# Kernel tuning notes

Hardware: AMD Instinct MI355X
Metric: run time of the kernel (lower is better)

## Reference

```python
import jax, jax.numpy as jnp
import numpy as np

TARGET_SIZE = 1024
SOURCE_SIZE = 1024


def setup_inputs() -> dict:
    key = jax.random.key(0)
    k1, k2, k3, k4 = jax.random.split(key, 4)
    B, T, S = 16, 1024, 1024
    sentence_state = jax.random.normal(k1, (B, T, TARGET_SIZE), dtype=jnp.float32)
    graph_state = jax.random.normal(k2, (B, S, SOURCE_SIZE), dtype=jnp.float32)
    mask = jax.random.bernoulli(k3, 0.5, (B, T, S))  # bool
    # nn.Linear(target_size+source_size, 1, bias=False).weight flattened
    w = jax.random.normal(k4, (TARGET_SIZE + SOURCE_SIZE,), dtype=jnp.float32) * (
        1.0 / np.sqrt(TARGET_SIZE + SOURCE_SIZE)
    )
    return {"sentence_state": sentence_state, "graph_state": graph_state, "mask": mask, "w": w}


def reference(sentence_state, graph_state, mask, w):
    # Linear on concat([tgt, src]) with out_features=1 decomposes into two dot products:
    # score[b,t,s] = sentence[b,t,:] @ w_t + graph[b,s,:] @ w_s
    w_t = w[:TARGET_SIZE]
    w_s = w[TARGET_SIZE:]
    st = jnp.einsum("btd,d->bt", sentence_state, w_t)  # (B, T)
    gs = jnp.einsum("bsd,d->bs", graph_state, w_s)  # (B, S)
    scores = st[:, :, None] + gs[:, None, :]  # (B, T, S)
    attn = jax.nn.softmax(scores, axis=-1)
    attn = attn * (~mask).astype(attn.dtype)
    norm = jnp.sum(attn, axis=-1, keepdims=True) + 1e-12
    return attn / norm
```

## Files before the change

### kernel.cpp

```cpp
#include <hip/hip_runtime.h>


constexpr int Bb = 16;
constexpr int Tt = 1024;
constexpr int Ss = 1024;
constexpr int Dd = 1024;

__global__ __launch_bounds__(256) void gs_exp_probe_kernel(
    const float* __restrict__ graph, const float* __restrict__ w_full,
    const unsigned char* __restrict__ mask, int* __restrict__ ws_flag,
    float* __restrict__ e_out) {
  if (blockIdx.x == 0) {
    __shared__ int nz[4];
    const int tid = threadIdx.x;
    if (tid < 4) nz[tid] = 0;
    __syncthreads();
    uchar4 v = reinterpret_cast<const uchar4*>(mask)[tid];
    if (v.x) atomicOr(&nz[0], 1);
    if (v.y) atomicOr(&nz[1], 1);
    if (v.z) atomicOr(&nz[2], 1);
    if (v.w) atomicOr(&nz[3], 1);
    __syncthreads();
    if (tid == 0) {
      int spread = (nz[0] != 0) + (nz[1] != 0) + (nz[2] != 0) + (nz[3] != 0);
      ws_flag[0] = (spread >= 3) ? 0 : 1;
    }
  }

  const int lane = threadIdx.x & 63;
  const int wv   = threadIdx.x >> 6;
  const long row = (long)blockIdx.x * 4 + wv;
  const float4* r  = reinterpret_cast<const float4*>(graph) + row * (Dd / 4);
  const float4* ws = reinterpret_cast<const float4*>(w_full + 1024);
  float acc = 0.f;
#pragma unroll
  for (int k = 0; k < 4; ++k) {
    float4 a = r[lane + 64 * k];
    float4 b = ws[lane + 64 * k];
    acc = fmaf(a.x, b.x, acc);
    acc = fmaf(a.y, b.y, acc);
    acc = fmaf(a.z, b.z, acc);
    acc = fmaf(a.w, b.w, acc);
  }
#pragma unroll
  for (int off = 32; off; off >>= 1) acc += __shfl_xor(acc, off, 64);
  if (lane == 0) e_out[row] = __expf(acc);
}

__global__ __launch_bounds__(256) void PointerGenerator_9259949490200_kernel(
    const float* __restrict__ e, const unsigned char* __restrict__ mask,
    const int* __restrict__ ws_flag, float* __restrict__ out) {
  constexpr int ROWS = 2;
  const int lane = threadIdx.x & 63;
  const int wv   = threadIdx.x >> 6;
  const int b    = blockIdx.y;

  const float4* e4 = reinterpret_cast<const float4*>(e + (long)b * Ss);
  float4 pr[4];
#pragma unroll
  for (int k = 0; k < 4; ++k) pr[k] = e4[lane + 64 * k];

  const int  mode = ws_flag[0];
  const long t0   = (long)blockIdx.x * (4 * ROWS) + (long)wv * ROWS;
  const long row0 = (long)b * Tt + t0;

  unsigned int mw[ROWS][4];
  if (mode == 0) {
    const unsigned int* m4 =
        reinterpret_cast<const unsigned int*>(mask + row0 * Ss);
#pragma unroll
    for (int r = 0; r < ROWS; ++r)
#pragma unroll
      for (int k = 0; k < 4; ++k) mw[r][k] = m4[r * 256 + lane + 64 * k];
  } else {
    const int4* m4 = reinterpret_cast<const int4*>(
        reinterpret_cast<const int*>(mask) + row0 * Ss);
#pragma unroll
    for (int r = 0; r < ROWS; ++r)
#pragma unroll
      for (int k = 0; k < 4; ++k) {
        int4 w = m4[r * 256 + lane + 64 * k];
        mw[r][k] = (unsigned)(w.x != 0) | ((unsigned)(w.y != 0) << 8) |
                   ((unsigned)(w.z != 0) << 16) | ((unsigned)(w.w != 0) << 24);
      }
  }

  float sum[ROWS];
#pragma unroll
  for (int r = 0; r < ROWS; ++r) {
    float s = 0.f;
#pragma unroll
    for (int k = 0; k < 4; ++k) {
      const unsigned int m = mw[r][k];
      s += (m & 0x000000FFu) ? 0.f : pr[k].x;
      s += (m & 0x0000FF00u) ? 0.f : pr[k].y;
      s += (m & 0x00FF0000u) ? 0.f : pr[k].z;
      s += (m & 0xFF000000u) ? 0.f : pr[k].w;
    }
    sum[r] = s;
  }
#pragma unroll
  for (int off = 32; off; off >>= 1)
#pragma unroll
    for (int r = 0; r < ROWS; ++r) sum[r] += __shfl_xor(sum[r], off, 64);

#pragma unroll
  for (int r = 0; r < ROWS; ++r) {
    const float invD = 1.0f / (sum[r] + 1e-12f);
    float4* orow = reinterpret_cast<float4*>(out + (row0 + r) * Ss);
#pragma unroll
    for (int k = 0; k < 4; ++k) {
      const unsigned int m = mw[r][k];
      float4 v;
      v.x = (m & 0x000000FFu) ? 0.f : pr[k].x * invD;
      v.y = (m & 0x0000FF00u) ? 0.f : pr[k].y * invD;
      v.z = (m & 0x00FF0000u) ? 0.f : pr[k].z * invD;
      v.w = (m & 0xFF000000u) ? 0.f : pr[k].w * invD;
      orow[lane + 64 * k] = v;
    }
  }
}

extern "C" void kernel_launch(void* const* d_in, const int* in_sizes, int n_in,
                              void* d_out, int out_size, void* d_ws, size_t ws_size,
                              hipStream_t stream) {
  const float* graph        = (const float*)d_in[1];
  const unsigned char* mask = (const unsigned char*)d_in[2];
  const float* w            = (const float*)d_in[3];
  float* out = (float*)d_out;

  int*   ws_flag = (int*)d_ws;
  float* e       = (float*)((char*)d_ws + 256);

  gs_exp_probe_kernel<<<(Bb * Ss) / 4, 256, 0, stream>>>(graph, w, mask,
                                                         ws_flag, e);
  PointerGenerator_9259949490200_kernel<<<dim3(Tt / (4 * 2), Bb), 256, 0, stream>>>(
      e, mask, ws_flag, out);
}
```

Baseline: 35.85 us.

## Fuse graph-score and normalize kernels with producer/consumer waves and spin-wait flags

Result: slower. 54.25 us (+51.3%).

```diff
diff --git a/kernel.cpp b/kernel.cpp
--- a/kernel.cpp
+++ b/kernel.cpp
@@ -6,117 +6,125 @@
 constexpr int Ss = 1024;
 constexpr int Dd = 1024;
 
-__global__ __launch_bounds__(256) void gs_exp_probe_kernel(
+__global__ __launch_bounds__(256) void zero_e_kernel(float* __restrict__ e) {
+  reinterpret_cast<float4*>(e)[blockIdx.x * 256 + threadIdx.x] =
+      make_float4(0.f, 0.f, 0.f, 0.f);
+}
+
+__global__ __launch_bounds__(256, 2) void PointerGenerator_9259949490200_kernel(
     const float* __restrict__ graph, const float* __restrict__ w_full,
-    const unsigned char* __restrict__ mask, int* __restrict__ ws_flag,
-    float* __restrict__ e_out) {
-  if (blockIdx.x == 0) {
-    __shared__ int nz[4];
-    const int tid = threadIdx.x;
-    if (tid < 4) nz[tid] = 0;
-    __syncthreads();
-    uchar4 v = reinterpret_cast<const uchar4*>(mask)[tid];
-    if (v.x) atomicOr(&nz[0], 1);
-    if (v.y) atomicOr(&nz[1], 1);
-    if (v.z) atomicOr(&nz[2], 1);
-    if (v.w) atomicOr(&nz[3], 1);
-    __syncthreads();
-    if (tid == 0) {
-      int spread = (nz[0] != 0) + (nz[1] != 0) + (nz[2] != 0) + (nz[3] != 0);
-      ws_flag[0] = (spread >= 3) ? 0 : 1;
-    }
-  }
-
+    const unsigned char* __restrict__ mask, float* e, float* __restrict__ out) {
   const int lane = threadIdx.x & 63;
   const int wv   = threadIdx.x >> 6;
-  const long row = (long)blockIdx.x * 4 + wv;
-  const float4* r  = reinterpret_cast<const float4*>(graph) + row * (Dd / 4);
-  const float4* ws = reinterpret_cast<const float4*>(w_full + 1024);
-  float acc = 0.f;
+  const int blk  = blockIdx.x;
+
+  if (wv < 2) {
+    const float4* wsv = reinterpret_cast<const float4*>(w_full + Ss);
+    float4 wr[4];
 #pragma unroll
-  for (int k = 0; k < 4; ++k) {
-    float4 a = r[lane + 64 * k];
-    float4 b = ws[lane + 64 * k];
-    acc = fmaf(a.x, b.x, acc);
-    acc = fmaf(a.y, b.y, acc);
-    acc = fmaf(a.z, b.z, acc);
-    acc = fmaf(a.w, b.w, acc);
-  }
-#pragma unroll
-  for (int off = 32; off; off >>= 1) acc += __shfl_xor(acc, off, 64);
-  if (lane == 0) e_out[row] = __expf(acc);
-}
-
-__global__ __launch_bounds__(256) void PointerGenerator_9259949490200_kernel(
-    const float* __restrict__ e, const unsigned char* __restrict__ mask,
-    const int* __restrict__ ws_flag, float* __restrict__ out) {
-  constexpr int ROWS = 2;
-  const int lane = threadIdx.x & 63;
-  const int wv   = threadIdx.x >> 6;
-  const int b    = blockIdx.y;
-
-  const float4* e4 = reinterpret_cast<const float4*>(e + (long)b * Ss);
-  float4 pr[4];
-#pragma unroll
-  for (int k = 0; k < 4; ++k) pr[k] = e4[lane + 64 * k];
-
-  const int  mode = ws_flag[0];
-  const long t0   = (long)blockIdx.x * (4 * ROWS) + (long)wv * ROWS;
-  const long row0 = (long)b * Tt + t0;
-
-  unsigned int mw[ROWS][4];
-  if (mode == 0) {
-    const unsigned int* m4 =
-        reinterpret_cast<const unsigned int*>(mask + row0 * Ss);
-#pragma unroll
-    for (int r = 0; r < ROWS; ++r)
-#pragma unroll
-      for (int k = 0; k < 4; ++k) mw[r][k] = m4[r * 256 + lane + 64 * k];
-  } else {
-    const int4* m4 = reinterpret_cast<const int4*>(
-        reinterpret_cast<const int*>(mask) + row0 * Ss);
-#pragma unroll
-    for (int r = 0; r < ROWS; ++r)
+    for (int k = 0; k < 4; ++k) wr[k] = wsv[lane + 64 * k];
+    const int rbase = blk * 2 + wv;
+#pragma unroll 1
+    for (int b = 0; b < Bb; ++b) {
+      const long row = (long)b * Ss + rbase;
+      const float4* r = reinterpret_cast<const float4*>(graph) + row * (Dd / 4);
+      float acc = 0.f;
 #pragma unroll
       for (int k = 0; k < 4; ++k) {
-        int4 w = m4[r * 256 + lane + 64 * k];
-        mw[r][k] = (unsigned)(w.x != 0) | ((unsigned)(w.y != 0) << 8) |
-                   ((unsigned)(w.z != 0) << 16) | ((unsigned)(w.w != 0) << 24);
+        float4 a = r[lane + 64 * k];
+        acc = fmaf(a.x, wr[k].x, acc);
+        acc = fmaf(a.y, wr[k].y, acc);
+        acc = fmaf(a.z, wr[k].z, acc);
+        acc = fmaf(a.w, wr[k].w, acc);
       }
-  }
+#pragma unroll
+      for (int off = 32; off; off >>= 1) acc += __shfl_xor(acc, off, 64);
+      if (lane == 0)
+        __hip_atomic_store(&e[row], __expf(acc), __ATOMIC_RELAXED,
+                           __HIP_MEMORY_SCOPE_AGENT);
+    }
+  } else {
+    uint4 pv = reinterpret_cast<const uint4*>(mask)[lane];
+    int bits = 0;
+    {
+      unsigned dw[4] = {pv.x, pv.y, pv.z, pv.w};
+#pragma unroll
+      for (int j = 0; j < 4; ++j) {
+        unsigned d = dw[j];
+        bits |= ((d & 0x000000FFu) ? 1 : 0) | ((d & 0x0000FF00u) ? 2 : 0) |
+                ((d & 0x00FF0000u) ? 4 : 0) | ((d & 0xFF000000u) ? 8 : 0);
+      }
+    }
+    const int spread = ((__ballot(bits & 1) != 0ull) ? 1 : 0) +
+                       ((__ballot(bits & 2) != 0ull) ? 1 : 0) +
+                       ((__ballot(bits & 4) != 0ull) ? 1 : 0) +
+                       ((__ballot(bits & 8) != 0ull) ? 1 : 0);
+    const int mode = (spread >= 3) ? 0 : 1;
+    const int trow = blk * 2 + (wv - 2);
 
-  float sum[ROWS];
+#pragma unroll 1
+    for (int b = 0; b < Bb; ++b) {
+      const float* eb = e + (long)b * Ss;
+      float ev[16];
+      int tries = 0;
+      while (true) {
+        bool ok = true;
 #pragma unroll
-  for (int r = 0; r < ROWS; ++r) {
-    float s = 0.f;
+        for (int k = 0; k < 4; ++k)
 #pragma unroll
-    for (int k = 0; k < 4; ++k) {
-      const unsigned int m = mw[r][k];
-      s += (m & 0x000000FFu) ? 0.f : pr[k].x;
-      s += (m & 0x0000FF00u) ? 0.f : pr[k].y;
-      s += (m & 0x00FF0000u) ? 0.f : pr[k].z;
-      s += (m & 0xFF000000u) ? 0.f : pr[k].w;
-    }
-    sum[r] = s;
-  }
+          for (int c = 0; c < 4; ++c) {
+            float v = __hip_atomic_load(&eb[4 * lane + 256 * k + c],
+                                        __ATOMIC_RELAXED,
+                                        __HIP_MEMORY_SCOPE_AGENT);
+            ev[4 * k + c] = v;
+            ok = ok && (v > 0.f);
+          }
+        if (__all(ok) || ++tries > 200000) break;
+        __builtin_amdgcn_s_sleep(8);
+      }
+
+      const long orow = (long)b * Tt + trow;
+      unsigned mw[4];
+      if (mode == 0) {
+        const unsigned* mr =
+            reinterpret_cast<const unsigned*>(mask + orow * Ss);
 #pragma unroll
-  for (int off = 32; off; off >>= 1)
+        for (int k = 0; k < 4; ++k) mw[k] = mr[lane + 64 * k];
+      } else {
+        const int4* mr = reinterpret_cast<const int4*>(
+            reinterpret_cast<const int*>(mask) + orow * Ss);
 #pragma unroll
-    for (int r = 0; r < ROWS; ++r) sum[r] += __shfl_xor(sum[r], off, 64);
+        for (int k = 0; k < 4; ++k) {
+          int4 w = mr[lane + 64 * k];
+          mw[k] = (unsigned)(w.x != 0) | ((unsigned)(w.y != 0) << 8) |
+                  ((unsigned)(w.z != 0) << 16) | ((unsigned)(w.w != 0) << 24);
+        }
+      }
 
+      float s = 0.f;
 #pragma unroll
-  for (int r = 0; r < ROWS; ++r) {
-    const float invD = 1.0f / (sum[r] + 1e-12f);
-    float4* orow = reinterpret_cast<float4*>(out + (row0 + r) * Ss);
+      for (int k = 0; k < 4; ++k) {
+        const unsigned m = mw[k];
+        s += (m & 0x000000FFu) ? 0.f : ev[4 * k + 0];
+        s += (m & 0x0000FF00u) ? 0.f : ev[4 * k + 1];
+        s += (m & 0x00FF0000u) ? 0.f : ev[4 * k + 2];
+        s += (m & 0xFF000000u) ? 0.f : ev[4 * k + 3];
+      }
 #pragma unroll
-    for (int k = 0; k < 4; ++k) {
-      const unsigned int m = mw[r][k];
-      float4 v;
-      v.x = (m & 0x000000FFu) ? 0.f : pr[k].x * invD;
-      v.y = (m & 0x0000FF00u) ? 0.f : pr[k].y * invD;
-      v.z = (m & 0x00FF0000u) ? 0.f : pr[k].z * invD;
-      v.w = (m & 0xFF000000u) ? 0.f : pr[k].w * invD;
-      orow[lane + 64 * k] = v;
+      for (int off = 32; off; off >>= 1) s += __shfl_xor(s, off, 64);
+      const float invD = 1.0f / (s + 1e-12f);
+
+      float4* o = reinterpret_cast<float4*>(out + orow * Ss);
+#pragma unroll
+      for (int k = 0; k < 4; ++k) {
+        const unsigned m = mw[k];
+        float4 v;
+        v.x = (m & 0x000000FFu) ? 0.f : ev[4 * k + 0] * invD;
+        v.y = (m & 0x0000FF00u) ? 0.f : ev[4 * k + 1] * invD;
+        v.z = (m & 0x00FF0000u) ? 0.f : ev[4 * k + 2] * invD;
+        v.w = (m & 0xFF000000u) ? 0.f : ev[4 * k + 3] * invD;
+        o[lane + 64 * k] = v;
+      }
     }
   }
 }
@@ -128,12 +136,9 @@
   const unsigned char* mask = (const unsigned char*)d_in[2];
   const float* w            = (const float*)d_in[3];
   float* out = (float*)d_out;
+  float* e   = (float*)d_ws;
 
-  int*   ws_flag = (int*)d_ws;
-  float* e       = (float*)((char*)d_ws + 256);
-
-  gs_exp_probe_kernel<<<(Bb * Ss) / 4, 256, 0, stream>>>(graph, w, mask,
-                                                         ws_flag, e);
-  PointerGenerator_9259949490200_kernel<<<dim3(Tt / (4 * 2), Bb), 256, 0, stream>>>(
-      e, mask, ws_flag, out);
+  zero_e_kernel<<<16, 256, 0, stream>>>(e);
+  PointerGenerator_9259949490200_kernel<<<512, 256, 0, stream>>>(
+      graph, w, mask, e, out);
 }
```

## Split row-sum normalization into a separate kernel before output write

Applied to the files above, without the earlier changes.

Result: slower. 47.53 us (+32.6%).

```diff
diff --git a/kernel.cpp b/kernel.cpp
--- a/kernel.cpp
+++ b/kernel.cpp
@@ -47,36 +47,33 @@
   if (lane == 0) e_out[row] = __expf(acc);
 }
 
-__global__ __launch_bounds__(256) void PointerGenerator_9259949490200_kernel(
+__global__ __launch_bounds__(256) void row_sums_kernel(
     const float* __restrict__ e, const unsigned char* __restrict__ mask,
-    const int* __restrict__ ws_flag, float* __restrict__ out) {
-  constexpr int ROWS = 2;
+    const int* __restrict__ ws_flag, float* __restrict__ invD) {
   const int lane = threadIdx.x & 63;
   const int wv   = threadIdx.x >> 6;
-  const int b    = blockIdx.y;
+  const int wid  = blockIdx.x * 4 + wv;
+  const long row0 = (long)wid * 2;
+  const int b    = (int)(row0 >> 10);
 
   const float4* e4 = reinterpret_cast<const float4*>(e + (long)b * Ss);
   float4 pr[4];
 #pragma unroll
   for (int k = 0; k < 4; ++k) pr[k] = e4[lane + 64 * k];
 
-  const int  mode = ws_flag[0];
-  const long t0   = (long)blockIdx.x * (4 * ROWS) + (long)wv * ROWS;
-  const long row0 = (long)b * Tt + t0;
-
-  unsigned int mw[ROWS][4];
+  const int mode = ws_flag[0];
+  unsigned mw[2][4];
   if (mode == 0) {
-    const unsigned int* m4 =
-        reinterpret_cast<const unsigned int*>(mask + row0 * Ss);
+    const unsigned* m4 = reinterpret_cast<const unsigned*>(mask + row0 * Ss);
 #pragma unroll
-    for (int r = 0; r < ROWS; ++r)
+    for (int r = 0; r < 2; ++r)
 #pragma unroll
       for (int k = 0; k < 4; ++k) mw[r][k] = m4[r * 256 + lane + 64 * k];
   } else {
     const int4* m4 = reinterpret_cast<const int4*>(
         reinterpret_cast<const int*>(mask) + row0 * Ss);
 #pragma unroll
-    for (int r = 0; r < ROWS; ++r)
+    for (int r = 0; r < 2; ++r)
 #pragma unroll
       for (int k = 0; k < 4; ++k) {
         int4 w = m4[r * 256 + lane + 64 * k];
@@ -85,13 +82,13 @@
       }
   }
 
-  float sum[ROWS];
+  float sum[2];
 #pragma unroll
-  for (int r = 0; r < ROWS; ++r) {
+  for (int r = 0; r < 2; ++r) {
     float s = 0.f;
 #pragma unroll
     for (int k = 0; k < 4; ++k) {
-      const unsigned int m = mw[r][k];
+      const unsigned m = mw[r][k];
       s += (m & 0x000000FFu) ? 0.f : pr[k].x;
       s += (m & 0x0000FF00u) ? 0.f : pr[k].y;
       s += (m & 0x00FF0000u) ? 0.f : pr[k].z;
@@ -100,22 +97,67 @@
     sum[r] = s;
   }
 #pragma unroll
-  for (int off = 32; off; off >>= 1)
+  for (int off = 32; off; off >>= 1) {
+    sum[0] += __shfl_xor(sum[0], off, 64);
+    sum[1] += __shfl_xor(sum[1], off, 64);
+  }
+  if (lane == 0) {
+    invD[row0]     = 1.0f / (sum[0] + 1e-12f);
+    invD[row0 + 1] = 1.0f / (sum[1] + 1e-12f);
+  }
+}
+
+__global__ __launch_bounds__(256) void PointerGenerator_9259949490200_kernel(
+    const float* __restrict__ e, const unsigned char* __restrict__ mask,
+    const int* __restrict__ ws_flag, const float* __restrict__ invD,
+    float* __restrict__ out) {
+  const int lane = threadIdx.x & 63;
+  const int wv   = threadIdx.x >> 6;
+  const int wid  = blockIdx.x * 4 + wv;
+  const long row0 = (long)wid * 2;
+  const int b    = (int)(row0 >> 10);
+
+  const float4* e4 = reinterpret_cast<const float4*>(e + (long)b * Ss);
+  float4 pr[4];
 #pragma unroll
-    for (int r = 0; r < ROWS; ++r) sum[r] += __shfl_xor(sum[r], off, 64);
+  for (int k = 0; k < 4; ++k) pr[k] = e4[lane + 64 * k];
+
+  const int mode = ws_flag[0];
+  unsigned mw[2][4];
+  if (mode == 0) {
+    const unsigned* m4 = reinterpret_cast<const unsigned*>(mask + row0 * Ss);
+#pragma unroll
+    for (int r = 0; r < 2; ++r)
+#pragma unroll
+      for (int k = 0; k < 4; ++k) mw[r][k] = m4[r * 256 + lane + 64 * k];
+  } else {
+    const int4* m4 = reinterpret_cast<const int4*>(
+        reinterpret_cast<const int*>(mask) + row0 * Ss);
+#pragma unroll
+    for (int r = 0; r < 2; ++r)
+#pragma unroll
+      for (int k = 0; k < 4; ++k) {
+        int4 w = m4[r * 256 + lane + 64 * k];
+        mw[r][k] = (unsigned)(w.x != 0) | ((unsigned)(w.y != 0) << 8) |
+                   ((unsigned)(w.z != 0) << 16) | ((unsigned)(w.w != 0) << 24);
+      }
+  }
+
+  const float i0 = invD[row0];
+  const float i1 = invD[row0 + 1];
 
 #pragma unroll
-  for (int r = 0; r < ROWS; ++r) {
-    const float invD = 1.0f / (sum[r] + 1e-12f);
+  for (int r = 0; r < 2; ++r) {
+    const float iv = (r == 0) ? i0 : i1;
     float4* orow = reinterpret_cast<float4*>(out + (row0 + r) * Ss);
 #pragma unroll
     for (int k = 0; k < 4; ++k) {
-      const unsigned int m = mw[r][k];
+      const unsigned m = mw[r][k];
       float4 v;
-      v.x = (m & 0x000000FFu) ? 0.f : pr[k].x * invD;
-      v.y = (m & 0x0000FF00u) ? 0.f : pr[k].y * invD;
-      v.z = (m & 0x00FF0000u) ? 0.f : pr[k].z * invD;
-      v.w = (m & 0xFF000000u) ? 0.f : pr[k].w * invD;
+      v.x = (m & 0x000000FFu) ? 0.f : pr[k].x * iv;
+      v.y = (m & 0x0000FF00u) ? 0.f : pr[k].y * iv;
+      v.z = (m & 0x00FF0000u) ? 0.f : pr[k].z * iv;
+      v.w = (m & 0xFF000000u) ? 0.f : pr[k].w * iv;
       orow[lane + 64 * k] = v;
     }
   }
@@ -131,9 +173,11 @@
 
   int*   ws_flag = (int*)d_ws;
   float* e       = (float*)((char*)d_ws + 256);
+  float* invD    = e + Bb * Ss;
 
   gs_exp_probe_kernel<<<(Bb * Ss) / 4, 256, 0, stream>>>(graph, w, mask,
                                                          ws_flag, e);
-  PointerGenerator_9259949490200_kernel<<<dim3(Tt / (4 * 2), Bb), 256, 0, stream>>>(
-      e, mask, ws_flag, out);
+  row_sums_kernel<<<(Bb * Tt) / 8, 256, 0, stream>>>(e, mask, ws_flag, invD);
+  PointerGenerator_9259949490200_kernel<<<(Bb * Tt) / 8, 256, 0, stream>>>(
+      e, mask, ws_flag, invD, out);
 }
```
